# Kernel optimization log

Measured on AMD Instinct MI355X. Metric: run time of the kernel, lower is better.

## Reference

```python
import jax, jax.numpy as jnp
import numpy as np

IMG_H, IMG_W = 512, 512
TILE_H, TILE_W = 64, 64
MARGIN = 0


def _cubrt(x):
    return jnp.sign(x) * jnp.abs(x) ** (1.0 / 3.0)


def _ssqrt(x):
    return jnp.sqrt(jnp.maximum(x, 0.0))


def _sacos(x):
    return jnp.arccos(jnp.clip(x, -1.0, 1.0))


def _solve_cubic(ax, ay, az):
    # roots of t^3 + ax t^2 + ay t + az = 0; returns (..., 2)
    ax2 = ax * ax
    p = ay - ax2 / 3.0
    p3 = p * p * p
    q = ax * (2.0 * ax2 - 9.0 * ay) / 27.0 + az
    d = q * q + 4.0 * p3 / 27.0
    sd = _ssqrt(d)
    root0 = _cubrt((sd - q) * 0.5) + _cubrt((-sd - q) * 0.5) - ax / 3.0
    p3s = jnp.where(jnp.abs(p3) > 1e-9, p3, 1e-9)
    v = _sacos(-_ssqrt(-27.0 / p3s) * q * 0.5) / 3.0
    m = jnp.cos(v)
    n = jnp.sin(v) * np.sqrt(3.0)
    sp = _ssqrt(-p / 3.0)
    root1 = (m + m) * sp - ax / 3.0
    root2 = (-n - m) * sp - ax / 3.0
    single = jnp.stack(jnp.broadcast_arrays(root0, root0), -1)
    double = jnp.stack([root1, root2], -1)
    return jnp.where(d[..., None] > 0, single, double)


def _bbox_mask(a, b, c, lw):
    # tile-granular culling mask (B,N,H,W); computed under no_grad in original
    a, b, c, lw = map(jax.lax.stop_gradient, (a, b, c, lw))
    SC = float(min(IMG_H, IMG_W))
    mi = jnp.minimum(a, c)
    ma = jnp.maximum(a, c)
    cond = jnp.any((b < mi) | (b > ma), axis=-1, keepdims=True)
    denom = a - 2.0 * b + c
    denom_ok = jnp.all(jnp.abs(denom) > 1e-9, axis=-1, keepdims=True)
    t = jnp.clip((a - b) / jnp.where(jnp.abs(denom) > 1e-9, denom, 1e-9), 0.0, 1.0)
    s = 1.0 - t
    qq = s * s * a + 2.0 * s * t * b + t * t * c  # extremum of the quadratic
    use_q = cond & denom_ok
    mi = jnp.where(use_q, jnp.minimum(mi, qq), mi)
    ma = jnp.where(use_q, jnp.maximum(ma, qq), ma)
    mg = jnp.floor(MARGIN + 3.0 * lw)[..., None]  # int() truncation, lw > 0
    lim = jnp.array([IMG_H, IMG_W], dtype=a.dtype)
    mi_px = jnp.clip(jnp.floor(mi * SC) - mg, 0.0, lim)  # (B,N,2) [y0,x0]
    ma_px = jnp.clip(jnp.ceil(ma * SC) + mg, 0.0, lim)   # (B,N,2) [y1,x1]
    ty = (jnp.arange(IMG_H) // TILE_H * TILE_H).astype(a.dtype)  # tile start per pixel row
    tx = (jnp.arange(IMG_W) // TILE_W * TILE_W).astype(a.dtype)
    my = (ma_px[..., 0:1] > ty) & (mi_px[..., 0:1] < ty + TILE_H)  # (B,N,H)
    mx = (ma_px[..., 1:2] > tx) & (mi_px[..., 1:2] < tx + TILE_W)  # (B,N,W)
    return my[..., :, None] & mx[..., None, :]


def _forward(a, b, c, lw, lc):
    mask = _bbox_mask(a, b, c, lw)
    H, W = IMG_H, IMG_W
    mn = float(min(H, W))
    yy, xx = jnp.meshgrid(jnp.linspace(0.0, H / mn, H), jnp.linspace(0.0, W / mn, W), indexing='ij')
    p = jnp.stack([yy, xx], -1).astype(a.dtype)  # (H,W,2)
    bb = b + 1e-5
    A = bb - a                      # (B,N,2)
    Bq = c - bb - A                 # (B,N,2)
    C = p[None, None] - a[:, :, None, None]  # (B,N,H,W,2)
    D = 2.0 * A[:, :, None, None]
    Bq4 = Bq[:, :, None, None]
    BdB = jnp.sum(Bq * Bq, -1)[:, :, None, None]  # (B,N,1,1)
    ca = (-3.0 * jnp.sum(A * Bq, -1)[:, :, None, None]) / -BdB
    cb = (jnp.sum(C * Bq4, -1) - 2.0 * jnp.sum(A * A, -1)[:, :, None, None]) / -BdB
    cc = jnp.sum(C * A[:, :, None, None], -1) / -BdB
    T = jnp.clip(_solve_cubic(ca, cb, cc), 0.0, 1.0)  # (B,N,H,W,2)
    d1 = (D + Bq4 * T[..., 0:1]) * T[..., 0:1] - C
    d2 = (D + Bq4 * T[..., 1:2]) * T[..., 1:2] - C
    dist = _ssqrt(jnp.minimum(jnp.sum(d1 * d1, -1), jnp.sum(d2 * d2, -1)))  # (B,N,H,W)
    lw4 = lw[:, :, None, None]
    lc4 = lc[:, :, None, None]
    inten = jax.nn.sigmoid((lw4 - dist) / lw4 * 6.0) * lc4
    return 1.0 - jnp.sum(jnp.where(mask, inten, 0.0), axis=1, keepdims=True)  # (B,1,H,W)


def setup_inputs() -> dict:
    key = jax.random.key(0)
    k0, k1, k2, k3, k4 = jax.random.split(key, 5)
    B, N = 1, 128
    a = jax.random.uniform(k0, (B, N, 2), dtype=jnp.float32)
    b = jax.random.uniform(k1, (B, N, 2), dtype=jnp.float32)
    c = jax.random.uniform(k2, (B, N, 2), dtype=jnp.float32)
    lw = jax.random.uniform(k3, (B, N), dtype=jnp.float32) * 0.01 + 0.003
    lc = jax.random.uniform(k4, (B, N), dtype=jnp.float32)
    return {'a': a, 'b': b, 'c': c, 'lw': lw, 'lc': lc}


def reference(a, b, c, lw, lc):
    return _forward(a, b, c, lw, lc)
```

## Files before the change

kernel.cpp:

```cpp
#include <hip/hip_runtime.h>
#include <math.h>

#define NSPL 128
#define SCALE 512.0f

__device__ __forceinline__ float fast_cbrt_pos(float x) {
    float r  = __builtin_amdgcn_exp2f(__builtin_amdgcn_logf(x) * (1.0f/3.0f));
    float r2 = r * r;
    r = fmaf(0.33333333f, fmaf(x, __builtin_amdgcn_rcpf(r2), -r), r);
    return (x < 1e-35f) ? 0.0f : r;
}

__device__ __forceinline__ float cos_small(float v) {
    const float v2 = v * v;
    float p = -2.7557319e-7f;
    p = fmaf(p, v2, 2.4801587e-5f);
    p = fmaf(p, v2, -1.3888889e-3f);
    p = fmaf(p, v2, 4.1666667e-2f);
    p = fmaf(p, v2, -0.5f);
    return fmaf(p, v2, 1.0f);
}
__device__ __forceinline__ float sin_small(float v) {
    const float v2 = v * v;
    float p = 2.7557319e-6f;
    p = fmaf(p, v2, -1.9841270e-4f);
    p = fmaf(p, v2, 8.3333333e-3f);
    p = fmaf(p, v2, -0.16666667f);
    return v * fmaf(p, v2, 1.0f);
}

__device__ __forceinline__ float eval_one(
    float py, float px, const float4 f0, const float4 f1,
    const float4 f2, const float4 lw4)
{
    const float Ay = f0.z, Ax = f0.w;
    const float By = f1.x, Bx = f1.y;
    const float ca27 = f1.z, ca3 = f1.w;
    const float twoax2 = f2.x, third = f2.y, cbK = f2.z, r_nB = f2.w;

    const float Cy = py - f0.x, Cx = px - f0.y;
    const float CdB = Cy*By + Cx*Bx;
    const float CdA = Cy*Ay + Cx*Ax;
    const float cb = (CdB - cbK) * r_nB;
    const float cc = CdA * r_nB;

    const float p_  = cb - third;
    const float p3  = p_ * p_ * p_;
    const float q   = fmaf(ca27, fmaf(-9.0f, cb, twoax2), cc);
    const float d   = fmaf(q, q, p3 * (4.0f/27.0f));

    const bool sgl = d > 0.0f;
    const float sd = __builtin_amdgcn_sqrtf(fmaxf(d, 0.0f));
    const float mm = (fabsf(q) + sd) * 0.5f;
    const float r  = fast_cbrt_pos(mm);
    const float sg = (q > 0.0f) ? -1.0f : 1.0f;
    const float r0 = fmaf(sg, fmaf(-p_ * 0.33333334f, __builtin_amdgcn_rcpf(r), r), -ca3);

    float T0 = r0, T1 = r0;
    const unsigned long long bd = __ballot(sgl);
    if (bd != ~0ull) {
        const float p3s = (fabsf(p3) > 1e-9f) ? p3 : 1e-9f;
        const float aarg = -sqrtf(fmaxf(-27.0f / p3s, 0.0f)) * q * 0.5f;
        const float v = acosf(fminf(fmaxf(aarg, -1.0f), 1.0f)) / 3.0f;
        const float m = cos_small(v);
        const float nn = sin_small(v) * 1.7320508075688772f;
        const float sp = sqrtf(fmaxf(-p_ / 3.0f, 0.0f));
        const float r1 = (m + m) * sp - ca3;
        const float r2 = (-nn - m) * sp - ca3;
        if (!sgl) { T0 = r1; T1 = r2; }
    }
    T0 = fminf(fmaxf(T0, 0.0f), 1.0f);
    T1 = fminf(fmaxf(T1, 0.0f), 1.0f);

    const float Dy = Ay + Ay, Dx = Ax + Ax;
    const float d1y = (Dy + By*T0)*T0 - Cy, d1x = (Dx + Bx*T0)*T0 - Cx;
    const float d2y = (Dy + By*T1)*T1 - Cy, d2x = (Dx + Bx*T1)*T1 - Cx;
    const float q1 = d1y*d1y + d1x*d1x;
    const float q2 = d2y*d2y + d2x*d2x;
    const float dist = __builtin_amdgcn_sqrtf(fminf(q1, q2));

    const float sarg = (lw4.z - dist) * lw4.y;
    const float e = __builtin_amdgcn_exp2f(sarg * -1.4426950408889634f);
    return lw4.x * __builtin_amdgcn_rcpf(1.0f + e);
}

__global__ __launch_bounds__(256) void spline_render(
    const float* __restrict__ ga, const float* __restrict__ gb,
    const float* __restrict__ gc, const float* __restrict__ glw,
    const float* __restrict__ glc, float* __restrict__ out)
{
    __shared__ float4 s_f0[NSPL], s_f1[NSPL], s_f2[NSPL], s_eb[NSPL];
    __shared__ float4 s_sa[NSPL], s_sb[NSPL], s_sc[NSPL];
    __shared__ float4 s_lw[NSPL];
    __shared__ int    s_wl[4][NSPL];

    const int t  = threadIdx.x;
    const int bx = blockIdx.x & 31;
    const int by = blockIdx.x >> 5;
    const float ty0 = (float)((by >> 2) << 6);
    const float tx0 = (float)((bx >> 2) << 6);

    if (t < NSPL) {
        const int n = t;
        const float ay  = ga[2*n],  ax  = ga[2*n+1];
        const float by_ = gb[2*n],  bx_ = gb[2*n+1];
        const float cy  = gc[2*n],  cx  = gc[2*n+1];
        const float w   = glw[n];

        float miy = fminf(ay, cy), may = fmaxf(ay, cy);
        float mix = fminf(ax, cx), maxx = fmaxf(ax, cx);
        bool cond = (by_ < miy) || (by_ > may) || (bx_ < mix) || (bx_ > maxx);
        float dny = ay - 2.0f*by_ + cy;
        float dnx = ax - 2.0f*bx_ + cx;
        bool dok = (fabsf(dny) > 1e-9f) && (fabsf(dnx) > 1e-9f);
        float tty = fminf(fmaxf((ay - by_) / ((fabsf(dny) > 1e-9f) ? dny : 1e-9f), 0.0f), 1.0f);
        float ttx = fminf(fmaxf((ax - bx_) / ((fabsf(dnx) > 1e-9f) ? dnx : 1e-9f), 0.0f), 1.0f);
        float sy = 1.0f - tty, sx = 1.0f - ttx;
        float qqy = sy*sy*ay + 2.0f*sy*tty*by_ + tty*tty*cy;
        float qqx = sx*sx*ax + 2.0f*sx*ttx*bx_ + ttx*ttx*cx;
        if (cond && dok) {
            miy = fminf(miy, qqy); may = fmaxf(may, qqy);
            mix = fminf(mix, qqx); maxx = fmaxf(maxx, qqx);
        }
        float mg = floorf(3.0f * w);
        float mi_py = fminf(fmaxf(floorf(miy*SCALE) - mg, 0.0f), 512.0f);
        float ma_py = fminf(fmaxf(ceilf (may*SCALE) + mg, 0.0f), 512.0f);
        float mi_px = fminf(fmaxf(floorf(mix*SCALE) - mg, 0.0f), 512.0f);
        float ma_px = fminf(fmaxf(ceilf (maxx*SCALE) + mg, 0.0f), 512.0f);
        bool flag = (ma_py > ty0) && (mi_py < ty0 + 64.0f)
                 && (ma_px > tx0) && (mi_px < tx0 + 64.0f);

        float bby = by_ + 1e-5f, bbx = bx_ + 1e-5f;
        float Ay = bby - ay, Ax = bbx - ax;
        float By = cy - bby - Ay, Bx = cx - bbx - Ax;
        float BdB = By*By + Bx*Bx;
        float nB  = -BdB;
        float AdB = Ay*By + Ax*Bx;
        float ca  = (-3.0f * AdB) / nB;
        float ax2 = ca * ca;
        s_f0[n] = make_float4(ay, ax, Ay, Ax);
        s_f1[n] = make_float4(By, Bx, ca / 27.0f, ca / 3.0f);
        s_f2[n] = make_float4(2.0f * ax2, ax2 / 3.0f,
                              2.0f * (Ay*Ay + Ax*Ax), 1.0f / nB);
        s_lw[n] = make_float4(glc[n], 6.0f / w, w, 0.0f);

        float E = fmaf(2.9f * 512.0f, w, 3.0f);
        s_eb[n] = flag ? make_float4(mi_py - E, ma_py + E, mi_px - E, ma_px + E)
                       : make_float4(1e30f, -1e30f, 1e30f, -1e30f);

        float q0y = ay * 511.0f,                                   q0x = ax * 511.0f;
        float q1y = (ay + 2.0f*Ay*0.25f + By*0.0625f) * 511.0f,    q1x = (ax + 2.0f*Ax*0.25f + Bx*0.0625f) * 511.0f;
        float q2y = (ay + Ay + By*0.25f) * 511.0f,                 q2x = (ax + Ax + Bx*0.25f) * 511.0f;
        float q3y = (ay + 2.0f*Ay*0.75f + By*0.5625f) * 511.0f,    q3x = (ax + 2.0f*Ax*0.75f + Bx*0.5625f) * 511.0f;
        float q4y = (ay + 2.0f*Ay + By) * 511.0f,                  q4x = (ax + 2.0f*Ax + Bx) * 511.0f;
        float dev = __builtin_amdgcn_sqrtf(BdB) * (511.0f / 64.0f);
        float R   = E + dev + 6.0f;
        s_sa[n] = make_float4(q0y, q0x, q1y, q1x);
        s_sb[n] = make_float4(q2y, q2x, q3y, q3x);
        s_sc[n] = make_float4(q4y, q4x, R * R, 0.0f);
    }
    __syncthreads();

    const int lane = t & 63;
    const int wv   = t >> 6;
    const int wx0 = (bx << 4) + ((wv & 1) << 3);
    const int wy0 = (by << 4) + ((wv >> 1) << 3);
    const float wy0f = (float)wy0, wx0f = (float)wx0;
    const float cyp = wy0f + 3.5f, cxp = wx0f + 3.5f;

    int cnt = 0;
    #pragma unroll
    for (int h = 0; h < 2; ++h) {
        const int n = (h << 6) + lane;
        const float4 eb = s_eb[n];
        bool keep = (eb.y > wy0f) && (eb.x < wy0f + 8.0f)
                 && (eb.w > wx0f) && (eb.z < wx0f + 8.0f);
        if (keep) {
            const float4 sa = s_sa[n];
            const float4 sb = s_sb[n];
            const float4 sc = s_sc[n];
            float best = 1e30f;
            float py0 = sa.x, px0 = sa.y;
            #pragma unroll
            for (int s = 0; s < 4; ++s) {
                const float py1 = (s == 0) ? sa.z : (s == 1) ? sb.x : (s == 2) ? sb.z : sc.x;
                const float px1 = (s == 0) ? sa.w : (s == 1) ? sb.y : (s == 2) ? sb.w : sc.y;
                const float vy = py1 - py0, vx = px1 - px0;
                const float wy = cyp - py0, wx = cxp - px0;
                const float vv = fmaxf(vy*vy + vx*vx, 1e-12f);
                const float tt = fminf(fmaxf((wy*vy + wx*vx) * __builtin_amdgcn_rcpf(vv), 0.0f), 1.0f);
                const float dy = wy - tt*vy, dx = wx - tt*vx;
                best = fminf(best, dy*dy + dx*dx);
                py0 = py1; px0 = px1;
            }
            keep = best <= sc.z;
        }
        const unsigned long long b = __ballot(keep);
        const int pos = cnt + __popcll(b & ((1ull << lane) - 1ull));
        if (keep) s_wl[wv][pos] = n;
        cnt += __popcll(b);
    }

    const int px_i = wx0 + (lane & 7);
    const int py_i = wy0 + (lane >> 3);
    const float py = (float)py_i * (1.0f / 511.0f);
    const float px = (float)px_i * (1.0f / 511.0f);

    float sum = 0.0f;
    int i = 0;
    for (; i + 3 <= cnt; i += 3) {
        const int n0 = s_wl[wv][i];
        const int n1 = s_wl[wv][i+1];
        const int n2 = s_wl[wv][i+2];
        const float c_0 = eval_one(py, px, s_f0[n0], s_f1[n0], s_f2[n0], s_lw[n0]);
        const float c_1 = eval_one(py, px, s_f0[n1], s_f1[n1], s_f2[n1], s_lw[n1]);
        const float c_2 = eval_one(py, px, s_f0[n2], s_f1[n2], s_f2[n2], s_lw[n2]);
        sum = ((sum + c_0) + c_1) + c_2;
    }
    for (; i < cnt; ++i) {
        const int n0 = s_wl[wv][i];
        sum += eval_one(py, px, s_f0[n0], s_f1[n0], s_f2[n0], s_lw[n0]);
    }

    out[py_i * 512 + px_i] = 1.0f - sum;
}

extern "C" void kernel_launch(void* const* d_in, const int* in_sizes, int n_in,
                              void* d_out, int out_size, void* d_ws, size_t ws_size,
                              hipStream_t stream) {
    const float* a  = (const float*)d_in[0];
    const float* b  = (const float*)d_in[1];
    const float* c  = (const float*)d_in[2];
    const float* lw = (const float*)d_in[3];
    const float* lc = (const float*)d_in[4];
    float* out = (float*)d_out;
    spline_render<<<dim3(1024), dim3(256), 0, stream>>>(a, b, c, lw, lc, out);
}
```

Baseline: 21.43 us.

## Split per-spline setup into a staging kernel and render from global workspace

```diff
diff --git a/kernel.cpp b/kernel.cpp
--- a/kernel.cpp
+++ b/kernel.cpp
@@ -84,101 +84,114 @@
     return lw4.x * __builtin_amdgcn_rcpf(1.0f + e);
 }
 
-__global__ __launch_bounds__(256) void spline_render(
+
+__global__ __launch_bounds__(128) void stage_k(
     const float* __restrict__ ga, const float* __restrict__ gb,
     const float* __restrict__ gc, const float* __restrict__ glw,
-    const float* __restrict__ glc, float* __restrict__ out)
+    const float* __restrict__ glc, float4* __restrict__ ws)
 {
-    __shared__ float4 s_f0[NSPL], s_f1[NSPL], s_f2[NSPL], s_eb[NSPL];
-    __shared__ float4 s_sa[NSPL], s_sb[NSPL], s_sc[NSPL];
-    __shared__ float4 s_lw[NSPL];
-    __shared__ int    s_wl[4][NSPL];
-
-    const int t  = threadIdx.x;
-    const int bx = blockIdx.x & 31;
-    const int by = blockIdx.x >> 5;
-    const float ty0 = (float)((by >> 2) << 6);
-    const float tx0 = (float)((bx >> 2) << 6);
-
-    if (t < NSPL) {
-        const int n = t;
-        const float ay  = ga[2*n],  ax  = ga[2*n+1];
-        const float by_ = gb[2*n],  bx_ = gb[2*n+1];
-        const float cy  = gc[2*n],  cx  = gc[2*n+1];
-        const float w   = glw[n];
-
-        float miy = fminf(ay, cy), may = fmaxf(ay, cy);
-        float mix = fminf(ax, cx), maxx = fmaxf(ax, cx);
-        bool cond = (by_ < miy) || (by_ > may) || (bx_ < mix) || (bx_ > maxx);
-        float dny = ay - 2.0f*by_ + cy;
-        float dnx = ax - 2.0f*bx_ + cx;
-        bool dok = (fabsf(dny) > 1e-9f) && (fabsf(dnx) > 1e-9f);
-        float tty = fminf(fmaxf((ay - by_) / ((fabsf(dny) > 1e-9f) ? dny : 1e-9f), 0.0f), 1.0f);
-        float ttx = fminf(fmaxf((ax - bx_) / ((fabsf(dnx) > 1e-9f) ? dnx : 1e-9f), 0.0f), 1.0f);
-        float sy = 1.0f - tty, sx = 1.0f - ttx;
-        float qqy = sy*sy*ay + 2.0f*sy*tty*by_ + tty*tty*cy;
-        float qqx = sx*sx*ax + 2.0f*sx*ttx*bx_ + ttx*ttx*cx;
-        if (cond && dok) {
-            miy = fminf(miy, qqy); may = fmaxf(may, qqy);
-            mix = fminf(mix, qqx); maxx = fmaxf(maxx, qqx);
-        }
-        float mg = floorf(3.0f * w);
-        float mi_py = fminf(fmaxf(floorf(miy*SCALE) - mg, 0.0f), 512.0f);
-        float ma_py = fminf(fmaxf(ceilf (may*SCALE) + mg, 0.0f), 512.0f);
-        float mi_px = fminf(fmaxf(floorf(mix*SCALE) - mg, 0.0f), 512.0f);
-        float ma_px = fminf(fmaxf(ceilf (maxx*SCALE) + mg, 0.0f), 512.0f);
-        bool flag = (ma_py > ty0) && (mi_py < ty0 + 64.0f)
-                 && (ma_px > tx0) && (mi_px < tx0 + 64.0f);
-
-        float bby = by_ + 1e-5f, bbx = bx_ + 1e-5f;
-        float Ay = bby - ay, Ax = bbx - ax;
-        float By = cy - bby - Ay, Bx = cx - bbx - Ax;
-        float BdB = By*By + Bx*Bx;
-        float nB  = -BdB;
-        float AdB = Ay*By + Ax*Bx;
-        float ca  = (-3.0f * AdB) / nB;
-        float ax2 = ca * ca;
-        s_f0[n] = make_float4(ay, ax, Ay, Ax);
-        s_f1[n] = make_float4(By, Bx, ca / 27.0f, ca / 3.0f);
-        s_f2[n] = make_float4(2.0f * ax2, ax2 / 3.0f,
-                              2.0f * (Ay*Ay + Ax*Ax), 1.0f / nB);
-        s_lw[n] = make_float4(glc[n], 6.0f / w, w, 0.0f);
-
-        float E = fmaf(2.9f * 512.0f, w, 3.0f);
-        s_eb[n] = flag ? make_float4(mi_py - E, ma_py + E, mi_px - E, ma_px + E)
-                       : make_float4(1e30f, -1e30f, 1e30f, -1e30f);
-
-        float q0y = ay * 511.0f,                                   q0x = ax * 511.0f;
-        float q1y = (ay + 2.0f*Ay*0.25f + By*0.0625f) * 511.0f,    q1x = (ax + 2.0f*Ax*0.25f + Bx*0.0625f) * 511.0f;
-        float q2y = (ay + Ay + By*0.25f) * 511.0f,                 q2x = (ax + Ax + Bx*0.25f) * 511.0f;
-        float q3y = (ay + 2.0f*Ay*0.75f + By*0.5625f) * 511.0f,    q3x = (ax + 2.0f*Ax*0.75f + Bx*0.5625f) * 511.0f;
-        float q4y = (ay + 2.0f*Ay + By) * 511.0f,                  q4x = (ax + 2.0f*Ax + Bx) * 511.0f;
-        float dev = __builtin_amdgcn_sqrtf(BdB) * (511.0f / 64.0f);
-        float R   = E + dev + 6.0f;
-        s_sa[n] = make_float4(q0y, q0x, q1y, q1x);
-        s_sb[n] = make_float4(q2y, q2x, q3y, q3x);
-        s_sc[n] = make_float4(q4y, q4x, R * R, 0.0f);
-    }
-    __syncthreads();
-
-    const int lane = t & 63;
-    const int wv   = t >> 6;
-    const int wx0 = (bx << 4) + ((wv & 1) << 3);
-    const int wy0 = (by << 4) + ((wv >> 1) << 3);
-    const float wy0f = (float)wy0, wx0f = (float)wx0;
+    const int n = threadIdx.x;
+    float4* g_mm = ws;
+    float4* g_eb = ws + 128;
+    float4* g_sa = ws + 256;
+    float4* g_sb = ws + 384;
+    float4* g_sc = ws + 512;
+    float4* g_f0 = ws + 640;
+    float4* g_f1 = ws + 768;
+    float4* g_f2 = ws + 896;
+    float4* g_lw = ws + 1024;
+
+    const float ay  = ga[2*n],  ax  = ga[2*n+1];
+    const float by_ = gb[2*n],  bx_ = gb[2*n+1];
+    const float cy  = gc[2*n],  cx  = gc[2*n+1];
+    const float w   = glw[n];
+
+    float miy = fminf(ay, cy), may = fmaxf(ay, cy);
+    float mix = fminf(ax, cx), maxx = fmaxf(ax, cx);
+    bool cond = (by_ < miy) || (by_ > may) || (bx_ < mix) || (bx_ > maxx);
+    float dny = ay - 2.0f*by_ + cy;
+    float dnx = ax - 2.0f*bx_ + cx;
+    bool dok = (fabsf(dny) > 1e-9f) && (fabsf(dnx) > 1e-9f);
+    float tty = fminf(fmaxf((ay - by_) / ((fabsf(dny) > 1e-9f) ? dny : 1e-9f), 0.0f), 1.0f);
+    float ttx = fminf(fmaxf((ax - bx_) / ((fabsf(dnx) > 1e-9f) ? dnx : 1e-9f), 0.0f), 1.0f);
+    float sy = 1.0f - tty, sx = 1.0f - ttx;
+    float qqy = sy*sy*ay + 2.0f*sy*tty*by_ + tty*tty*cy;
+    float qqx = sx*sx*ax + 2.0f*sx*ttx*bx_ + ttx*ttx*cx;
+    if (cond && dok) {
+        miy = fminf(miy, qqy); may = fmaxf(may, qqy);
+        mix = fminf(mix, qqx); maxx = fmaxf(maxx, qqx);
+    }
+    float mg = floorf(3.0f * w);
+    float mi_py = fminf(fmaxf(floorf(miy*SCALE) - mg, 0.0f), 512.0f);
+    float ma_py = fminf(fmaxf(ceilf (may*SCALE) + mg, 0.0f), 512.0f);
+    float mi_px = fminf(fmaxf(floorf(mix*SCALE) - mg, 0.0f), 512.0f);
+    float ma_px = fminf(fmaxf(ceilf (maxx*SCALE) + mg, 0.0f), 512.0f);
+    g_mm[n] = make_float4(mi_py, ma_py, mi_px, ma_px);
+
+    float bby = by_ + 1e-5f, bbx = bx_ + 1e-5f;
+    float Ay = bby - ay, Ax = bbx - ax;
+    float By = cy - bby - Ay, Bx = cx - bbx - Ax;
+    float BdB = By*By + Bx*Bx;
+    float nB  = -BdB;
+    float AdB = Ay*By + Ax*Bx;
+    float ca  = (-3.0f * AdB) / nB;
+    float ax2 = ca * ca;
+    g_f0[n] = make_float4(ay, ax, Ay, Ax);
+    g_f1[n] = make_float4(By, Bx, ca / 27.0f, ca / 3.0f);
+    g_f2[n] = make_float4(2.0f * ax2, ax2 / 3.0f,
+                          2.0f * (Ay*Ay + Ax*Ax), 1.0f / nB);
+    g_lw[n] = make_float4(glc[n], 6.0f / w, w, 0.0f);
+
+    float E = fmaf(2.9f * 512.0f, w, 3.0f);
+    g_eb[n] = make_float4(mi_py - E, ma_py + E, mi_px - E, ma_px + E);
+
+    float q0y = ay * 511.0f,                                   q0x = ax * 511.0f;
+    float q1y = (ay + 2.0f*Ay*0.25f + By*0.0625f) * 511.0f,    q1x = (ax + 2.0f*Ax*0.25f + Bx*0.0625f) * 511.0f;
+    float q2y = (ay + Ay + By*0.25f) * 511.0f,                 q2x = (ax + Ax + Bx*0.25f) * 511.0f;
+    float q3y = (ay + 2.0f*Ay*0.75f + By*0.5625f) * 511.0f,    q3x = (ax + 2.0f*Ax*0.75f + Bx*0.5625f) * 511.0f;
+    float q4y = (ay + 2.0f*Ay + By) * 511.0f,                  q4x = (ax + 2.0f*Ax + Bx) * 511.0f;
+    float dev = __builtin_amdgcn_sqrtf(BdB) * (511.0f / 64.0f);
+    float R   = E + dev + 6.0f;
+    g_sa[n] = make_float4(q0y, q0x, q1y, q1x);
+    g_sb[n] = make_float4(q2y, q2x, q3y, q3x);
+    g_sc[n] = make_float4(q4y, q4x, R * R, 0.0f);
+}
+
+__global__ __launch_bounds__(64) void render_k(
+    const float4* __restrict__ ws, float* __restrict__ out)
+{
+    const float4* g_mm = ws;
+    const float4* g_eb = ws + 128;
+    const float4* g_sa = ws + 256;
+    const float4* g_sb = ws + 384;
+    const float4* g_sc = ws + 512;
+    const float4* g_f0 = ws + 640;
+    const float4* g_f1 = ws + 768;
+    const float4* g_f2 = ws + 896;
+    const float4* g_lw = ws + 1024;
+
+    __shared__ int s_wl[NSPL];
+    const int lane = threadIdx.x;
+    const int rx = blockIdx.x & 63, ry = blockIdx.x >> 6;
+    const float wy0f = (float)(ry << 3), wx0f = (float)(rx << 3);
+    const float ty0 = (float)((ry >> 3) << 6);
+    const float tx0 = (float)((rx >> 3) << 6);
     const float cyp = wy0f + 3.5f, cxp = wx0f + 3.5f;
 
     int cnt = 0;
     #pragma unroll
     for (int h = 0; h < 2; ++h) {
         const int n = (h << 6) + lane;
-        const float4 eb = s_eb[n];
-        bool keep = (eb.y > wy0f) && (eb.x < wy0f + 8.0f)
+        const float4 mm = g_mm[n];
+        const float4 eb = g_eb[n];
+        bool keep = (mm.y > ty0) && (mm.x < ty0 + 64.0f)
+                 && (mm.w > tx0) && (mm.z < tx0 + 64.0f)
+                 && (eb.y > wy0f) && (eb.x < wy0f + 8.0f)
                  && (eb.w > wx0f) && (eb.z < wx0f + 8.0f);
         if (keep) {
-            const float4 sa = s_sa[n];
-            const float4 sb = s_sb[n];
-            const float4 sc = s_sc[n];
+            const float4 sa = g_sa[n];
+            const float4 sb = g_sb[n];
+            const float4 sc = g_sc[n];
             float best = 1e30f;
             float py0 = sa.x, px0 = sa.y;
             #pragma unroll
@@ -197,29 +210,30 @@
         }
         const unsigned long long b = __ballot(keep);
         const int pos = cnt + __popcll(b & ((1ull << lane) - 1ull));
-        if (keep) s_wl[wv][pos] = n;
+        if (keep) s_wl[pos] = n;
         cnt += __popcll(b);
     }
-
-    const int px_i = wx0 + (lane & 7);
-    const int py_i = wy0 + (lane >> 3);
+    __syncthreads();
+
+    const int px_i = (rx << 3) + (lane & 7);
+    const int py_i = (ry << 3) + (lane >> 3);
     const float py = (float)py_i * (1.0f / 511.0f);
     const float px = (float)px_i * (1.0f / 511.0f);
 
     float sum = 0.0f;
     int i = 0;
     for (; i + 3 <= cnt; i += 3) {
-        const int n0 = s_wl[wv][i];
-        const int n1 = s_wl[wv][i+1];
-        const int n2 = s_wl[wv][i+2];
-        const float c_0 = eval_one(py, px, s_f0[n0], s_f1[n0], s_f2[n0], s_lw[n0]);
-        const float c_1 = eval_one(py, px, s_f0[n1], s_f1[n1], s_f2[n1], s_lw[n1]);
-        const float c_2 = eval_one(py, px, s_f0[n2], s_f1[n2], s_f2[n2], s_lw[n2]);
+        const int n0 = s_wl[i];
+        const int n1 = s_wl[i+1];
+        const int n2 = s_wl[i+2];
+        const float c_0 = eval_one(py, px, g_f0[n0], g_f1[n0], g_f2[n0], g_lw[n0]);
+        const float c_1 = eval_one(py, px, g_f0[n1], g_f1[n1], g_f2[n1], g_lw[n1]);
+        const float c_2 = eval_one(py, px, g_f0[n2], g_f1[n2], g_f2[n2], g_lw[n2]);
         sum = ((sum + c_0) + c_1) + c_2;
     }
     for (; i < cnt; ++i) {
-        const int n0 = s_wl[wv][i];
-        sum += eval_one(py, px, s_f0[n0], s_f1[n0], s_f2[n0], s_lw[n0]);
+        const int n0 = s_wl[i];
+        sum += eval_one(py, px, g_f0[n0], g_f1[n0], g_f2[n0], g_lw[n0]);
     }
 
     out[py_i * 512 + px_i] = 1.0f - sum;
@@ -234,5 +248,8 @@
     const float* lw = (const float*)d_in[3];
     const float* lc = (const float*)d_in[4];
     float* out = (float*)d_out;
-    spline_render<<<dim3(1024), dim3(256), 0, stream>>>(a, b, c, lw, lc, out);
-}
+    float4* ws = (float4*)d_ws;
+
+    stage_k<<<dim3(1), dim3(128), 0, stream>>>(a, b, c, lw, lc, ws);
+    render_k<<<dim3(4096), dim3(64), 0, stream>>>(ws, out);
+}
```

After: 28.08 us. 31.0% more time.
